# Performance work log

Hardware: AMD Instinct MI355X
Metric: run time of the kernel (lower is better)

## Reference

```python
import jax, jax.numpy as jnp
import numpy as np

B, D, LC, LQ = 64, 128, 1024, 128
NEG = -1e30


def setup_inputs() -> dict:
    key = jax.random.key(0)
    k1, k2, k3 = jax.random.split(key, 3)
    lim = float(np.sqrt(1.0 / D))
    return {
        "C": jax.random.normal(k1, (B, D, LC), dtype=jnp.float32),
        "Q": jax.random.normal(k2, (B, D, LQ), dtype=jnp.float32),
        "cmask": jnp.ones((B, LC), dtype=jnp.float32),
        "qmask": jnp.ones((B, LQ), dtype=jnp.float32),
        "w": jax.random.uniform(k3, (3 * D,), dtype=jnp.float32, minval=-lim, maxval=lim),
    }


def reference(C, Q, cmask, qmask, w):
    # C: [B, D, Lc], Q: [B, D, Lq] -> transpose to [B, L, D] as in the torch module
    Ct = jnp.swapaxes(C, 1, 2)  # [B, Lc, D]
    Qt = jnp.swapaxes(Q, 1, 2)  # [B, Lq, D]
    d = Ct.shape[-1]
    # Trilinear decomposition of the per-step concat([Qi, C, Q*C]) . w loop:
    # S[b,c,q] = Qt[b,q] . w_q + Ct[b,c] . w_c + (Ct[b,c] * w_m) . Qt[b,q]
    w_q, w_c, w_m = w[:d], w[d:2 * d], w[2 * d:]
    s_q = Qt @ w_q                                   # [B, Lq]
    s_c = Ct @ w_c                                   # [B, Lc]
    s_m = jnp.einsum("bcd,bqd->bcq", Ct * w_m, Qt)   # [B, Lc, Lq]
    S = s_m + s_c[:, :, None] + s_q[:, None, :]      # [B, Lc, Lq]

    S1 = jax.nn.softmax(S + (1.0 - qmask)[:, None, :] * NEG, axis=2)
    S2 = jax.nn.softmax(S + (1.0 - cmask)[:, :, None] * NEG, axis=1)

    A = jnp.einsum("bcq,bqd->bcd", S1, Qt)           # [B, Lc, D]
    S12 = jnp.einsum("bcq,bkq->bck", S1, S2)         # [B, Lc, Lc]
    Bt = jnp.einsum("bck,bkd->bcd", S12, Ct)         # [B, Lc, D]

    out = jnp.concatenate([Ct, A, Ct * A, Ct * Bt], axis=2)  # [B, Lc, 4D]
    # dropout is identity in eval mode
    return jnp.swapaxes(out, 1, 2)                   # [B, 4D, Lc]
```

## Files before the change

kernel.cpp:

```cpp
#include <hip/hip_runtime.h>
#include <cstdint>
#include <cstddef>

#define B_  64
#define D_  128
#define LC_ 1024
#define LQ_ 128
#define NEGV (-1e30f)
#define NINF (-3.402823466e38f)

typedef short s16x8 __attribute__((ext_vector_type(8)));
typedef float f32x4 __attribute__((ext_vector_type(4)));

__device__ __forceinline__ unsigned short f2bf(float x) {
    union { float f; unsigned u; } v; v.f = x;
    unsigned r = v.u + 0x7fffu + ((v.u >> 16) & 1u);
    return (unsigned short)(r >> 16);
}

__global__ __launch_bounds__(256) void kQ(const float* __restrict__ Q,
                                          const float* __restrict__ w,
                                          unsigned short* __restrict__ Qt,
                                          unsigned short* __restrict__ Qb,
                                          float* __restrict__ sq_g) {
    __shared__ float tile[32][33];
    __shared__ float wq_l[128];
    __shared__ float red[8][32];
    int t = threadIdx.x;
    int b = blockIdx.y, q0 = blockIdx.x * 32;
    if (t < 128) wq_l[t] = w[t];
    __syncthreads();
    float sqp = 0.f;
    int qq = t & 31, db = t >> 5;
    for (int ch = 0; ch < 4; ch++) {
#pragma unroll
        for (int i = 0; i < 4; i++) {
            int dl = db * 4 + i;
            float v = Q[((size_t)(b * D_ + ch * 32 + dl)) * LQ_ + q0 + qq];
            tile[dl][qq] = v;
            sqp += v * wq_l[ch * 32 + dl];
        }
        __syncthreads();
        {
            int q2 = t >> 3, ds = (t & 7) * 4;
            ushort4 o;
            o.x = f2bf(tile[ds + 0][q2]);
            o.y = f2bf(tile[ds + 1][q2]);
            o.z = f2bf(tile[ds + 2][q2]);
            o.w = f2bf(tile[ds + 3][q2]);
            *(ushort4*)&Qt[((size_t)(b * LQ_ + q0 + q2)) * D_ + ch * 32 + ds] = o;
        }
        {
            int d2 = t >> 3, qs = (t & 7) * 4;
            ushort4 o;
            o.x = f2bf(tile[d2][qs + 0]);
            o.y = f2bf(tile[d2][qs + 1]);
            o.z = f2bf(tile[d2][qs + 2]);
            o.w = f2bf(tile[d2][qs + 3]);
            *(ushort4*)&Qb[((size_t)(b * D_ + ch * 32 + d2)) * LQ_ + q0 + qs] = o;
        }
        __syncthreads();
    }
    red[db][qq] = sqp;
    __syncthreads();
    if (t < 32) {
        float s = 0.f;
#pragma unroll
        for (int j = 0; j < 8; j++) s += red[j][t];
        sq_g[b * LQ_ + q0 + t] = s;
    }
}

__global__ __launch_bounds__(256) void kS(const float* __restrict__ C,
                                          const unsigned short* __restrict__ Qt,
                                          const float* __restrict__ w,
                                          const float* __restrict__ sq_g,
                                          const float* __restrict__ cmask,
                                          const float* __restrict__ qmask,
                                          unsigned short* __restrict__ S1b,
                                          float* __restrict__ pmax_g,
                                          float* __restrict__ psum_g,
                                          float* __restrict__ T2p) {
    __shared__ unsigned short CW[128 * 136];
    __shared__ unsigned short Tg[128 * 136];
    __shared__ float4 red4[8][32];
    __shared__ float wc_l[128], wm_l[128], sq_l[128], cmv_l[128], qmv_l[128], sc_l[128];

    int t = threadIdx.x;
    int b = blockIdx.y, c0 = blockIdx.x * 128;

    int g = t >> 5, c4 = t & 31;
    float4 v[16];
    {
        const float4* Cb = (const float4*)(C + (size_t)b * D_ * LC_ + c0);
#pragma unroll
        for (int j = 0; j < 16; j++) {
            int d = j * 8 + g;
            v[j] = Cb[(size_t)d * (LC_ / 4) + c4];
        }
    }
    if (t < 128) {
        wc_l[t] = w[D_ + t];
        wm_l[t] = w[2 * D_ + t];
        sq_l[t] = sq_g[b * LQ_ + t];
        cmv_l[t] = (1.0f - cmask[b * LC_ + c0 + t]) * NEGV;
        qmv_l[t] = (1.0f - qmask[b * LQ_ + t]) * NEGV;
    }
    __syncthreads();

    {
        float4 scp = {0.f, 0.f, 0.f, 0.f};
#pragma unroll
        for (int j = 0; j < 16; j++) {
            int d = j * 8 + g;
            float wcv = wc_l[d], wmv = wm_l[d];
            scp.x += v[j].x * wcv;
            scp.y += v[j].y * wcv;
            scp.z += v[j].z * wcv;
            scp.w += v[j].w * wcv;
            ushort4 o;
            o.x = f2bf(v[j].x * wmv);
            o.y = f2bf(v[j].y * wmv);
            o.z = f2bf(v[j].z * wmv);
            o.w = f2bf(v[j].w * wmv);
            *(ushort4*)&CW[d * 136 + c4 * 4] = o;
        }
        red4[g][c4] = scp;
    }
    __syncthreads();
    if (t < 128) {
        float s = 0.f;
#pragma unroll
        for (int gg = 0; gg < 8; gg++) {
            const float* rp = (const float*)&red4[gg][t >> 2];
            s += rp[t & 3];
        }
        sc_l[t] = s;
    }
    __syncthreads();

    int wv = t >> 6, l = t & 63, quad = l >> 4, lp = l & 15;
    int w32 = wv * 32;
    f32x4 zero = {0.f, 0.f, 0.f, 0.f};
    f32x4 acc[2][8];
#pragma unroll
    for (int mc = 0; mc < 2; mc++)
#pragma unroll
        for (int qt = 0; qt < 8; qt++) acc[mc][qt] = zero;

#pragma unroll
    for (int ks = 0; ks < 4; ks++) {
        s16x8 a[2], bb[8];
#pragma unroll
        for (int mc = 0; mc < 2; mc++) {
            s16x8 av;
#pragma unroll
            for (int e = 0; e < 8; e++)
                av[e] = (short)CW[(ks * 32 + quad * 8 + e) * 136 + w32 + mc * 16 + lp];
            a[mc] = av;
        }
#pragma unroll
        for (int qt = 0; qt < 8; qt++)
            bb[qt] = *(const s16x8*)&Qt[((size_t)(b * LQ_ + qt * 16 + lp)) * D_ + ks * 32 + quad * 8];
#pragma unroll
        for (int mc = 0; mc < 2; mc++)
#pragma unroll
            for (int qt = 0; qt < 8; qt++)
                acc[mc][qt] = __builtin_amdgcn_mfma_f32_16x16x32_bf16(a[mc], bb[qt], acc[mc][qt], 0, 0, 0);
    }
#pragma unroll
    for (int mc = 0; mc < 2; mc++)
#pragma unroll
        for (int qt = 0; qt < 8; qt++)
#pragma unroll
            for (int i = 0; i < 4; i++)
                acc[mc][qt][i] += sc_l[w32 + mc * 16 + quad * 4 + i] + sq_l[qt * 16 + lp];

    float qmv_r[8];
#pragma unroll
    for (int qt = 0; qt < 8; qt++) qmv_r[qt] = qmv_l[qt * 16 + lp];

    float rm_r[2][4], ri_r[2][4], gs_r[2][4];
#pragma unroll
    for (int mc = 0; mc < 2; mc++)
#pragma unroll
        for (int i = 0; i < 4; i++) {
            int row = w32 + mc * 16 + quad * 4 + i;
            float m = NINF;
#pragma unroll
            for (int qt = 0; qt < 8; qt++) m = fmaxf(m, acc[mc][qt][i] + qmv_r[qt]);
#pragma unroll
            for (int off = 1; off < 16; off <<= 1) m = fmaxf(m, __shfl_xor(m, off, 64));
            float s = 0.f;
#pragma unroll
            for (int qt = 0; qt < 8; qt++) s += __expf(acc[mc][qt][i] + qmv_r[qt] - m);
#pragma unroll
            for (int off = 1; off < 16; off <<= 1) s += __shfl_xor(s, off, 64);
            rm_r[mc][i] = m;
            ri_r[mc][i] = 1.0f / s;
            gs_r[mc][i] = s * __expf(m + cmv_l[row]);
        }

    float cmv_r[2][4];
#pragma unroll
    for (int mc = 0; mc < 2; mc++)
#pragma unroll
        for (int i = 0; i < 4; i++) cmv_r[mc][i] = cmv_l[w32 + mc * 16 + quad * 4 + i];
    int chunk = blockIdx.x * 4 + wv;
#pragma unroll
    for (int qt = 0; qt < 8; qt++) {
        float cm = NINF;
#pragma unroll
        for (int mc = 0; mc < 2; mc++)
#pragma unroll
            for (int i = 0; i < 4; i++) cm = fmaxf(cm, acc[mc][qt][i] + cmv_r[mc][i]);
        cm = fmaxf(cm, __shfl_xor(cm, 16, 64));
        cm = fmaxf(cm, __shfl_xor(cm, 32, 64));
        float cs = 0.f;
#pragma unroll
        for (int mc = 0; mc < 2; mc++)
#pragma unroll
            for (int i = 0; i < 4; i++) cs += __expf(acc[mc][qt][i] + cmv_r[mc][i] - cm);
        cs += __shfl_xor(cs, 16, 64);
        cs += __shfl_xor(cs, 32, 64);
        if (l < 16) {
            pmax_g[((size_t)(b * 32 + chunk)) * LQ_ + qt * 16 + lp] = cm;
            psum_g[((size_t)(b * 32 + chunk)) * LQ_ + qt * 16 + lp] = cs;
        }
    }

    __syncthreads();
#pragma unroll
    for (int mc = 0; mc < 2; mc++)
#pragma unroll
        for (int qt = 0; qt < 8; qt++)
#pragma unroll
            for (int i = 0; i < 4; i++) {
                int row = w32 + mc * 16 + quad * 4 + i;
                int q = qt * 16 + lp;
                float s1 = __expf(acc[mc][qt][i] + qmv_r[qt] - rm_r[mc][i]) * ri_r[mc][i];
                CW[row * 136 + q] = f2bf(s1);
                Tg[q * 136 + row] = f2bf(s1 * gs_r[mc][i]);
            }
    __syncthreads();

    {
        int row = t >> 1, qh = (t & 1) * 64;
        const uint4* src = (const uint4*)&CW[row * 136 + qh];
        uint4* dst = (uint4*)&S1b[((size_t)(b * LC_ + c0 + row)) * LQ_ + qh];
#pragma unroll
        for (int j = 0; j < 8; j++) dst[j] = src[j];
    }

    f32x4 acc2[2][8];
#pragma unroll
    for (int mc = 0; mc < 2; mc++)
#pragma unroll
        for (int nt = 0; nt < 8; nt++) acc2[mc][nt] = zero;
#pragma unroll
    for (int ks = 0; ks < 4; ks++) {
        s16x8 a2[2], bb[8];
#pragma unroll
        for (int m = 0; m < 2; m++) {
            int d = w32 + m * 16 + lp;
            const float4* p = (const float4*)&C[((size_t)(b * D_ + d)) * LC_ + c0 + ks * 32 + quad * 8];
            float4 v0 = p[0], v1 = p[1];
            unsigned short* pp = (unsigned short*)&a2[m];
            pp[0] = f2bf(v0.x); pp[1] = f2bf(v0.y); pp[2] = f2bf(v0.z); pp[3] = f2bf(v0.w);
            pp[4] = f2bf(v1.x); pp[5] = f2bf(v1.y); pp[6] = f2bf(v1.z); pp[7] = f2bf(v1.w);
        }
#pragma unroll
        for (int nt = 0; nt < 8; nt++)
            bb[nt] = *(const s16x8*)&Tg[(nt * 16 + lp) * 136 + ks * 32 + quad * 8];
#pragma unroll
        for (int m = 0; m < 2; m++)
#pragma unroll
            for (int nt = 0; nt < 8; nt++)
                acc2[m][nt] = __builtin_amdgcn_mfma_f32_16x16x32_bf16(a2[m], bb[nt], acc2[m][nt], 0, 0, 0);
    }
    size_t base = ((size_t)(blockIdx.x * B_ + b)) * ((size_t)D_ * LQ_);
#pragma unroll
    for (int mc = 0; mc < 2; mc++)
#pragma unroll
        for (int i = 0; i < 4; i++) {
            int d = w32 + mc * 16 + quad * 4 + i;
#pragma unroll
            for (int nt = 0; nt < 8; nt++)
                T2p[base + (size_t)d * LQ_ + nt * 16 + lp] = acc2[mc][nt][i];
        }
}

__global__ __launch_bounds__(128) void k2b(const float* __restrict__ pmax,
                                           const float* __restrict__ psum,
                                           float* __restrict__ hq_g,
                                           float* __restrict__ ci_g) {
    int q = threadIdx.x, b = blockIdx.x;
    float m = NINF;
    for (int j = 0; j < 32; j++) m = fmaxf(m, pmax[((size_t)(b * 32 + j)) * LQ_ + q]);
    float s = 0.f;
    for (int j = 0; j < 32; j++)
        s += psum[((size_t)(b * 32 + j)) * LQ_ + q] * __expf(pmax[((size_t)(b * 32 + j)) * LQ_ + q] - m);
    hq_g[b * LQ_ + q] = __expf(-m);
    ci_g[b * LQ_ + q] = 1.0f / s;
}

__global__ __launch_bounds__(256) void k3b(const float* __restrict__ T2p,
                                           const float* __restrict__ hq_g,
                                           const float* __restrict__ ci_g,
                                           unsigned short* __restrict__ T2b) {
    int idx = blockIdx.x * 256 + threadIdx.x;
    const size_t N = (size_t)B_ * D_ * LQ_;
    int b = idx >> 14, q = idx & 127;
    float s = 0.f;
#pragma unroll
    for (int j = 0; j < 8; j++) s += T2p[(size_t)j * N + idx];
    T2b[idx] = f2bf(s * hq_g[b * LQ_ + q] * ci_g[b * LQ_ + q]);
}

__global__ __launch_bounds__(256) void kC_out(const float* __restrict__ C,
                                              const unsigned short* __restrict__ Qb,
                                              const unsigned short* __restrict__ T2b,
                                              const unsigned short* __restrict__ S1b,
                                              float* __restrict__ out) {
    int t = threadIdx.x;
    int b = blockIdx.y, c0 = blockIdx.x * 64;
    int wv = t >> 6, l = t & 63, quad = l >> 4, lp = l & 15;
    int w32 = wv * 32;
    f32x4 zero = {0.f, 0.f, 0.f, 0.f};
    f32x4 accA[2][4], accB[2][4];
#pragma unroll
    for (int mc = 0; mc < 2; mc++)
#pragma unroll
        for (int nt = 0; nt < 4; nt++) { accA[mc][nt] = zero; accB[mc][nt] = zero; }

#pragma unroll
    for (int ks = 0; ks < 4; ks++) {
        s16x8 aq[2], at[2], bb[4];
        aq[0] = *(const s16x8*)&Qb[((size_t)(b * D_ + w32 + lp)) * LQ_ + ks * 32 + quad * 8];
        aq[1] = *(const s16x8*)&Qb[((size_t)(b * D_ + w32 + 16 + lp)) * LQ_ + ks * 32 + quad * 8];
        at[0] = *(const s16x8*)&T2b[((size_t)(b * D_ + w32 + lp)) * LQ_ + ks * 32 + quad * 8];
        at[1] = *(const s16x8*)&T2b[((size_t)(b * D_ + w32 + 16 + lp)) * LQ_ + ks * 32 + quad * 8];
#pragma unroll
        for (int nt = 0; nt < 4; nt++)
            bb[nt] = *(const s16x8*)&S1b[((size_t)(b * LC_ + c0 + nt * 16 + lp)) * LQ_ + ks * 32 + quad * 8];
#pragma unroll
        for (int mc = 0; mc < 2; mc++)
#pragma unroll
            for (int nt = 0; nt < 4; nt++) {
                accA[mc][nt] = __builtin_amdgcn_mfma_f32_16x16x32_bf16(aq[mc], bb[nt], accA[mc][nt], 0, 0, 0);
                accB[mc][nt] = __builtin_amdgcn_mfma_f32_16x16x32_bf16(at[mc], bb[nt], accB[mc][nt], 0, 0, 0);
            }
    }
    const size_t DL = (size_t)D_ * LC_;
#pragma unroll
    for (int mc = 0; mc < 2; mc++)
#pragma unroll
        for (int i = 0; i < 4; i++) {
            int d = w32 + mc * 16 + quad * 4 + i;
            const float* Crow = C + ((size_t)(b * D_ + d)) * LC_ + c0;
            size_t ob = ((size_t)(b * 4 * D_ + d)) * LC_ + c0;
#pragma unroll
            for (int nt = 0; nt < 4; nt++) {
                int c = nt * 16 + lp;
                float cv = Crow[c];
                float a = accA[mc][nt][i];
                float bt = accB[mc][nt][i];
                out[ob + c] = cv;
                out[ob + DL + c] = a;
                out[ob + 2 * DL + c] = cv * a;
                out[ob + 3 * DL + c] = cv * bt;
            }
        }
}

extern "C" void kernel_launch(void* const* d_in, const int* in_sizes, int n_in,
                              void* d_out, int out_size, void* d_ws, size_t ws_size,
                              hipStream_t stream) {
    const float* C     = (const float*)d_in[0];
    const float* Q     = (const float*)d_in[1];
    const float* cmask = (const float*)d_in[2];
    const float* qmask = (const float*)d_in[3];
    const float* w     = (const float*)d_in[4];
    float* out = (float*)d_out;

    unsigned short* us = (unsigned short*)d_ws;
    unsigned short* S1b = us;
    unsigned short* Qt  = S1b + (size_t)B_ * LC_ * LQ_;
    unsigned short* Qb  = Qt  + (size_t)B_ * LQ_ * D_;
    unsigned short* T2b = Qb  + (size_t)B_ * D_ * LQ_;
    float* fp = (float*)(T2b + (size_t)B_ * D_ * LQ_);
    float* T2p    = fp;
    float* pmax_g = T2p + (size_t)8 * B_ * D_ * LQ_;
    float* psum_g = pmax_g + (size_t)B_ * 32 * LQ_;
    float* sq_g   = psum_g + (size_t)B_ * 32 * LQ_;
    float* hq_g   = sq_g + (size_t)B_ * LQ_;
    float* ci_g   = hq_g + (size_t)B_ * LQ_;

    kQ<<<dim3(LQ_ / 32, B_), 256, 0, stream>>>(Q, w, Qt, Qb, sq_g);
    kS<<<dim3(LC_ / 128, B_), 256, 0, stream>>>(C, Qt, w, sq_g, cmask, qmask,
                                                S1b, pmax_g, psum_g, T2p);
    k2b<<<dim3(B_), 128, 0, stream>>>(pmax_g, psum_g, hq_g, ci_g);
    k3b<<<dim3(B_ * D_ * LQ_ / 256), 256, 0, stream>>>(T2p, hq_g, ci_g, T2b);
    kC_out<<<dim3(LC_ / 64, B_), 256, 0, stream>>>(C, Qb, T2b, S1b, out);
}
```

Before: 241.5 us.

## Swizzle CW LDS layout, cache softmax exps, transpose output GEMM for vector stores

Applies an XOR swizzle to the CW shared-memory tile on both the write and the column-gather read, to cut LDS bank conflicts. Stores the row-softmax exponentials back into the accumulators so the exp is computed once instead of twice. Restructures kC_out so each wave owns 16 context columns across all 128 D rows, with S1 as the A operand. The MFMA output then lands as 4 consecutive c values per lane, which allows float4 loads of C and float4 stores to all four output planes. The cost is more register pressure, since each wave now holds 16 accumulators and 16 B fragments, and the wider per-lane reads of Qb and T2b.

Result: slower. 250.6 us (+3.8%).

```diff
diff --git a/kernel.cpp b/kernel.cpp
--- a/kernel.cpp
+++ b/kernel.cpp
@@ -123,7 +123,7 @@
             o.y = f2bf(v[j].y * wmv);
             o.z = f2bf(v[j].z * wmv);
             o.w = f2bf(v[j].w * wmv);
-            *(ushort4*)&CW[d * 136 + c4 * 4] = o;
+            *(ushort4*)&CW[d * 136 + ((c4 ^ (j & 7)) << 2)] = o;
         }
         red4[g][c4] = scp;
     }
@@ -151,12 +151,15 @@
 #pragma unroll
     for (int ks = 0; ks < 4; ks++) {
         s16x8 a[2], bb[8];
+        int x3 = (ks * 4 + quad) & 7;
 #pragma unroll
         for (int mc = 0; mc < 2; mc++) {
             s16x8 av;
+            int c = w32 + mc * 16 + lp;
+            int cb = ((c >> 2) ^ x3) << 2, clo = c & 3;
 #pragma unroll
             for (int e = 0; e < 8; e++)
-                av[e] = (short)CW[(ks * 32 + quad * 8 + e) * 136 + w32 + mc * 16 + lp];
+                av[e] = (short)CW[(ks * 32 + quad * 8 + e) * 136 + cb + clo];
             a[mc] = av;
         }
 #pragma unroll
@@ -179,33 +182,25 @@
     float qmv_r[8];
 #pragma unroll
     for (int qt = 0; qt < 8; qt++) qmv_r[qt] = qmv_l[qt * 16 + lp];
-
-    float rm_r[2][4], ri_r[2][4], gs_r[2][4];
+    float cmv_r[2][4];
+#pragma unroll
+    for (int mc = 0; mc < 2; mc++)
+#pragma unroll
+        for (int i = 0; i < 4; i++) cmv_r[mc][i] = cmv_l[w32 + mc * 16 + quad * 4 + i];
+
+    float rm_r[2][4];
 #pragma unroll
     for (int mc = 0; mc < 2; mc++)
 #pragma unroll
         for (int i = 0; i < 4; i++) {
-            int row = w32 + mc * 16 + quad * 4 + i;
             float m = NINF;
 #pragma unroll
             for (int qt = 0; qt < 8; qt++) m = fmaxf(m, acc[mc][qt][i] + qmv_r[qt]);
 #pragma unroll
             for (int off = 1; off < 16; off <<= 1) m = fmaxf(m, __shfl_xor(m, off, 64));
-            float s = 0.f;
-#pragma unroll
-            for (int qt = 0; qt < 8; qt++) s += __expf(acc[mc][qt][i] + qmv_r[qt] - m);
-#pragma unroll
-            for (int off = 1; off < 16; off <<= 1) s += __shfl_xor(s, off, 64);
             rm_r[mc][i] = m;
-            ri_r[mc][i] = 1.0f / s;
-            gs_r[mc][i] = s * __expf(m + cmv_l[row]);
-        }
-
-    float cmv_r[2][4];
-#pragma unroll
-    for (int mc = 0; mc < 2; mc++)
-#pragma unroll
-        for (int i = 0; i < 4; i++) cmv_r[mc][i] = cmv_l[w32 + mc * 16 + quad * 4 + i];
+        }
+
     int chunk = blockIdx.x * 4 + wv;
 #pragma unroll
     for (int qt = 0; qt < 8; qt++) {
@@ -229,6 +224,24 @@
         }
     }
 
+    float ri_r[2][4], gs_r[2][4];
+#pragma unroll
+    for (int mc = 0; mc < 2; mc++)
+#pragma unroll
+        for (int i = 0; i < 4; i++) {
+            float s = 0.f;
+#pragma unroll
+            for (int qt = 0; qt < 8; qt++) {
+                float e = __expf(acc[mc][qt][i] + qmv_r[qt] - rm_r[mc][i]);
+                acc[mc][qt][i] = e;
+                s += e;
+            }
+#pragma unroll
+            for (int off = 1; off < 16; off <<= 1) s += __shfl_xor(s, off, 64);
+            ri_r[mc][i] = 1.0f / s;
+            gs_r[mc][i] = s * __expf(rm_r[mc][i] + cmv_r[mc][i]);
+        }
+
     __syncthreads();
 #pragma unroll
     for (int mc = 0; mc < 2; mc++)
@@ -238,7 +251,7 @@
             for (int i = 0; i < 4; i++) {
                 int row = w32 + mc * 16 + quad * 4 + i;
                 int q = qt * 16 + lp;
-                float s1 = __expf(acc[mc][qt][i] + qmv_r[qt] - rm_r[mc][i]) * ri_r[mc][i];
+                float s1 = acc[mc][qt][i] * ri_r[mc][i];
                 CW[row * 136 + q] = f2bf(s1);
                 Tg[q * 136 + row] = f2bf(s1 * gs_r[mc][i]);
             }
@@ -325,52 +338,41 @@
     int t = threadIdx.x;
     int b = blockIdx.y, c0 = blockIdx.x * 64;
     int wv = t >> 6, l = t & 63, quad = l >> 4, lp = l & 15;
-    int w32 = wv * 32;
+    int cw = c0 + wv * 16;
     f32x4 zero = {0.f, 0.f, 0.f, 0.f};
-    f32x4 accA[2][4], accB[2][4];
-#pragma unroll
-    for (int mc = 0; mc < 2; mc++)
-#pragma unroll
-        for (int nt = 0; nt < 4; nt++) { accA[mc][nt] = zero; accB[mc][nt] = zero; }
+    f32x4 accA[8], accB[8];
+#pragma unroll
+    for (int nt = 0; nt < 8; nt++) { accA[nt] = zero; accB[nt] = zero; }
 
 #pragma unroll
     for (int ks = 0; ks < 4; ks++) {
-        s16x8 aq[2], at[2], bb[4];
-        aq[0] = *(const s16x8*)&Qb[((size_t)(b * D_ + w32 + lp)) * LQ_ + ks * 32 + quad * 8];
-        aq[1] = *(const s16x8*)&Qb[((size_t)(b * D_ + w32 + 16 + lp)) * LQ_ + ks * 32 + quad * 8];
-        at[0] = *(const s16x8*)&T2b[((size_t)(b * D_ + w32 + lp)) * LQ_ + ks * 32 + quad * 8];
-        at[1] = *(const s16x8*)&T2b[((size_t)(b * D_ + w32 + 16 + lp)) * LQ_ + ks * 32 + quad * 8];
-#pragma unroll
-        for (int nt = 0; nt < 4; nt++)
-            bb[nt] = *(const s16x8*)&S1b[((size_t)(b * LC_ + c0 + nt * 16 + lp)) * LQ_ + ks * 32 + quad * 8];
-#pragma unroll
-        for (int mc = 0; mc < 2; mc++)
-#pragma unroll
-            for (int nt = 0; nt < 4; nt++) {
-                accA[mc][nt] = __builtin_amdgcn_mfma_f32_16x16x32_bf16(aq[mc], bb[nt], accA[mc][nt], 0, 0, 0);
-                accB[mc][nt] = __builtin_amdgcn_mfma_f32_16x16x32_bf16(at[mc], bb[nt], accB[mc][nt], 0, 0, 0);
-            }
+        s16x8 a = *(const s16x8*)&S1b[((size_t)(b * LC_ + cw + lp)) * LQ_ + ks * 32 + quad * 8];
+        s16x8 bq[8], bt[8];
+#pragma unroll
+        for (int nt = 0; nt < 8; nt++) {
+            bq[nt] = *(const s16x8*)&Qb[((size_t)(b * D_ + nt * 16 + lp)) * LQ_ + ks * 32 + quad * 8];
+            bt[nt] = *(const s16x8*)&T2b[((size_t)(b * D_ + nt * 16 + lp)) * LQ_ + ks * 32 + quad * 8];
+        }
+#pragma unroll
+        for (int nt = 0; nt < 8; nt++) {
+            accA[nt] = __builtin_amdgcn_mfma_f32_16x16x32_bf16(a, bq[nt], accA[nt], 0, 0, 0);
+            accB[nt] = __builtin_amdgcn_mfma_f32_16x16x32_bf16(a, bt[nt], accB[nt], 0, 0, 0);
+        }
     }
     const size_t DL = (size_t)D_ * LC_;
-#pragma unroll
-    for (int mc = 0; mc < 2; mc++)
-#pragma unroll
-        for (int i = 0; i < 4; i++) {
-            int d = w32 + mc * 16 + quad * 4 + i;
-            const float* Crow = C + ((size_t)(b * D_ + d)) * LC_ + c0;
-            size_t ob = ((size_t)(b * 4 * D_ + d)) * LC_ + c0;
-#pragma unroll
-            for (int nt = 0; nt < 4; nt++) {
-                int c = nt * 16 + lp;
-                float cv = Crow[c];
-                float a = accA[mc][nt][i];
-                float bt = accB[mc][nt][i];
-                out[ob + c] = cv;
-                out[ob + DL + c] = a;
-                out[ob + 2 * DL + c] = cv * a;
-                out[ob + 3 * DL + c] = cv * bt;
-            }
-        }
+    int cc = cw + quad * 4;
+#pragma unroll
+    for (int nt = 0; nt < 8; nt++) {
+        int d = nt * 16 + lp;
+        const f32x4 cv = *(const f32x4*)&C[((size_t)(b * D_ + d)) * LC_ + cc];
+        f32x4 av = accA[nt], bv = accB[nt];
+        f32x4 ca = cv * av, cb = cv * bv;
+        size_t ob = ((size_t)(b * 4 * D_ + d)) * LC_ + cc;
+        *(f32x4*)&out[ob] = cv;
+        *(f32x4*)&out[ob + DL] = av;
+        *(f32x4*)&out[ob + 2 * DL] = ca;
+        *(f32x4*)&out[ob + 3 * DL] = cb;
+    }
 }
 
 extern "C" void kernel_launch(void* const* d_in, const int* in_sizes, int n_in,
```

## Fuse Q preprocessing into score kernel and merge reduction kernels

Applied to the files above, without the earlier changes.

The standalone Q transpose/bf16 kernel is removed: each score block now loads Q itself, transposes it through shared memory, computes s_q locally, and reuses the LDS buffers. The two small reduction kernels are merged into one that computes per-query column scales and reduces the T2 partials. The output kernel converts Q to bf16 on the fly and uses 128-column tiles. It also adds an XOR swizzle on the CW shared buffer, caches exponentials instead of recomputing them, and sets a two-blocks-per-CU launch bound. This cuts two launches and the Qt/Qb workspace traffic, at the cost of every score block redoing Q's transpose and conversion.

Measured after the change: 219.1 us. 9.3% less time.

```diff
diff --git a/kernel.cpp b/kernel.cpp
--- a/kernel.cpp
+++ b/kernel.cpp
@@ -18,78 +18,24 @@
     return (unsigned short)(r >> 16);
 }
 
-__global__ __launch_bounds__(256) void kQ(const float* __restrict__ Q,
-                                          const float* __restrict__ w,
-                                          unsigned short* __restrict__ Qt,
-                                          unsigned short* __restrict__ Qb,
-                                          float* __restrict__ sq_g) {
-    __shared__ float tile[32][33];
-    __shared__ float wq_l[128];
-    __shared__ float red[8][32];
+__global__ __launch_bounds__(256, 2) void k1(const float* __restrict__ C,
+                                             const float* __restrict__ Q,
+                                             const float* __restrict__ cmask,
+                                             const float* __restrict__ qmask,
+                                             const float* __restrict__ w,
+                                             unsigned short* __restrict__ S1b,
+                                             float* __restrict__ pmax_g,
+                                             float* __restrict__ psum_g,
+                                             float* __restrict__ T2p) {
+    __shared__ unsigned short CW[128 * 136];
+    __shared__ unsigned short QT[128 * 136];
+    __shared__ float4 red4[8][32];
+    __shared__ float wc_l[128], wm_l[128], cmv_l[128], qmv_l[128], sc_l[128], sq_l[128];
+
     int t = threadIdx.x;
-    int b = blockIdx.y, q0 = blockIdx.x * 32;
-    if (t < 128) wq_l[t] = w[t];
-    __syncthreads();
-    float sqp = 0.f;
-    int qq = t & 31, db = t >> 5;
-    for (int ch = 0; ch < 4; ch++) {
-#pragma unroll
-        for (int i = 0; i < 4; i++) {
-            int dl = db * 4 + i;
-            float v = Q[((size_t)(b * D_ + ch * 32 + dl)) * LQ_ + q0 + qq];
-            tile[dl][qq] = v;
-            sqp += v * wq_l[ch * 32 + dl];
-        }
-        __syncthreads();
-        {
-            int q2 = t >> 3, ds = (t & 7) * 4;
-            ushort4 o;
-            o.x = f2bf(tile[ds + 0][q2]);
-            o.y = f2bf(tile[ds + 1][q2]);
-            o.z = f2bf(tile[ds + 2][q2]);
-            o.w = f2bf(tile[ds + 3][q2]);
-            *(ushort4*)&Qt[((size_t)(b * LQ_ + q0 + q2)) * D_ + ch * 32 + ds] = o;
-        }
-        {
-            int d2 = t >> 3, qs = (t & 7) * 4;
-            ushort4 o;
-            o.x = f2bf(tile[d2][qs + 0]);
-            o.y = f2bf(tile[d2][qs + 1]);
-            o.z = f2bf(tile[d2][qs + 2]);
-            o.w = f2bf(tile[d2][qs + 3]);
-            *(ushort4*)&Qb[((size_t)(b * D_ + ch * 32 + d2)) * LQ_ + q0 + qs] = o;
-        }
-        __syncthreads();
-    }
-    red[db][qq] = sqp;
-    __syncthreads();
-    if (t < 32) {
-        float s = 0.f;
-#pragma unroll
-        for (int j = 0; j < 8; j++) s += red[j][t];
-        sq_g[b * LQ_ + q0 + t] = s;
-    }
-}
-
-__global__ __launch_bounds__(256) void kS(const float* __restrict__ C,
-                                          const unsigned short* __restrict__ Qt,
-                                          const float* __restrict__ w,
-                                          const float* __restrict__ sq_g,
-                                          const float* __restrict__ cmask,
-                                          const float* __restrict__ qmask,
-                                          unsigned short* __restrict__ S1b,
-                                          float* __restrict__ pmax_g,
-                                          float* __restrict__ psum_g,
-                                          float* __restrict__ T2p) {
-    __shared__ unsigned short CW[128 * 136];
-    __shared__ unsigned short Tg[128 * 136];
-    __shared__ float4 red4[8][32];
-    __shared__ float wc_l[128], wm_l[128], sq_l[128], cmv_l[128], qmv_l[128], sc_l[128];
-
-    int t = threadIdx.x;
-    int b = blockIdx.y, c0 = blockIdx.x * 128;
-
+    int b = blockIdx.y, ct = blockIdx.x, c0 = ct * 128;
     int g = t >> 5, c4 = t & 31;
+
     float4 v[16];
     {
         const float4* Cb = (const float4*)(C + (size_t)b * D_ * LC_ + c0);
@@ -99,14 +45,49 @@
             v[j] = Cb[(size_t)d * (LC_ / 4) + c4];
         }
     }
+    float* wq_l = (float*)red4;
     if (t < 128) {
+        wq_l[t] = w[t];
         wc_l[t] = w[D_ + t];
         wm_l[t] = w[2 * D_ + t];
-        sq_l[t] = sq_g[b * LQ_ + t];
         cmv_l[t] = (1.0f - cmask[b * LC_ + c0 + t]) * NEGV;
         qmv_l[t] = (1.0f - qmask[b * LQ_ + t]) * NEGV;
     }
     __syncthreads();
+
+    {
+        float* CWf = (float*)CW;
+        int qq = t >> 1, ph = t & 1;
+        float sqv = 0.f;
+#pragma unroll
+        for (int h = 0; h < 2; h++) {
+#pragma unroll
+            for (int j = 0; j < 8; j++) {
+                int idx = j * 256 + t;
+                int r = idx >> 5, cc = idx & 31;
+                float4 qv = *(const float4*)&Q[((size_t)(b * D_ + h * 64 + r)) * LQ_ + cc * 4];
+                *(float4*)&CWf[r * 132 + cc * 4] = qv;
+            }
+            __syncthreads();
+            unsigned short u[32];
+#pragma unroll
+            for (int k = 0; k < 32; k++) {
+                float val = CWf[(ph * 32 + k) * 132 + qq];
+                sqv += val * wq_l[h * 64 + ph * 32 + k];
+                u[k] = f2bf(val);
+            }
+#pragma unroll
+            for (int k4 = 0; k4 < 8; k4++) {
+                ushort4 o;
+                o.x = u[k4 * 4 + 0]; o.y = u[k4 * 4 + 1];
+                o.z = u[k4 * 4 + 2]; o.w = u[k4 * 4 + 3];
+                *(ushort4*)&QT[qq * 136 + h * 64 + ph * 32 + k4 * 4] = o;
+            }
+            __syncthreads();
+        }
+        sqv += __shfl_xor(sqv, 1, 64);
+        if (ph == 0) sq_l[qq] = sqv;
+    }
 
     {
         float4 scp = {0.f, 0.f, 0.f, 0.f};
@@ -123,7 +104,7 @@
             o.y = f2bf(v[j].y * wmv);
             o.z = f2bf(v[j].z * wmv);
             o.w = f2bf(v[j].w * wmv);
-            *(ushort4*)&CW[d * 136 + c4 * 4] = o;
+            *(ushort4*)&CW[d * 136 + ((c4 ^ (j & 7)) << 2)] = o;
         }
         red4[g][c4] = scp;
     }
@@ -151,17 +132,20 @@
 #pragma unroll
     for (int ks = 0; ks < 4; ks++) {
         s16x8 a[2], bb[8];
+        int x3 = (ks * 4 + quad) & 7;
 #pragma unroll
         for (int mc = 0; mc < 2; mc++) {
             s16x8 av;
+            int c = w32 + mc * 16 + lp;
+            int cb = ((c >> 2) ^ x3) << 2, clo = c & 3;
 #pragma unroll
             for (int e = 0; e < 8; e++)
-                av[e] = (short)CW[(ks * 32 + quad * 8 + e) * 136 + w32 + mc * 16 + lp];
+                av[e] = (short)CW[(ks * 32 + quad * 8 + e) * 136 + cb + clo];
             a[mc] = av;
         }
 #pragma unroll
         for (int qt = 0; qt < 8; qt++)
-            bb[qt] = *(const s16x8*)&Qt[((size_t)(b * LQ_ + qt * 16 + lp)) * D_ + ks * 32 + quad * 8];
+            bb[qt] = *(const s16x8*)&QT[(qt * 16 + lp) * 136 + ks * 32 + quad * 8];
 #pragma unroll
         for (int mc = 0; mc < 2; mc++)
 #pragma unroll
@@ -179,34 +163,26 @@
     float qmv_r[8];
 #pragma unroll
     for (int qt = 0; qt < 8; qt++) qmv_r[qt] = qmv_l[qt * 16 + lp];
-
-    float rm_r[2][4], ri_r[2][4], gs_r[2][4];
+    float cmv_r[2][4];
+#pragma unroll
+    for (int mc = 0; mc < 2; mc++)
+#pragma unroll
+        for (int i = 0; i < 4; i++) cmv_r[mc][i] = cmv_l[w32 + mc * 16 + quad * 4 + i];
+
+    float rm_r[2][4];
 #pragma unroll
     for (int mc = 0; mc < 2; mc++)
 #pragma unroll
         for (int i = 0; i < 4; i++) {
-            int row = w32 + mc * 16 + quad * 4 + i;
             float m = NINF;
 #pragma unroll
             for (int qt = 0; qt < 8; qt++) m = fmaxf(m, acc[mc][qt][i] + qmv_r[qt]);
 #pragma unroll
             for (int off = 1; off < 16; off <<= 1) m = fmaxf(m, __shfl_xor(m, off, 64));
-            float s = 0.f;
-#pragma unroll
-            for (int qt = 0; qt < 8; qt++) s += __expf(acc[mc][qt][i] + qmv_r[qt] - m);
-#pragma unroll
-            for (int off = 1; off < 16; off <<= 1) s += __shfl_xor(s, off, 64);
             rm_r[mc][i] = m;
-            ri_r[mc][i] = 1.0f / s;
-            gs_r[mc][i] = s * __expf(m + cmv_l[row]);
-        }
-
-    float cmv_r[2][4];
-#pragma unroll
-    for (int mc = 0; mc < 2; mc++)
-#pragma unroll
-        for (int i = 0; i < 4; i++) cmv_r[mc][i] = cmv_l[w32 + mc * 16 + quad * 4 + i];
-    int chunk = blockIdx.x * 4 + wv;
+        }
+
+    int chunk = ct * 4 + wv;
 #pragma unroll
     for (int qt = 0; qt < 8; qt++) {
         float cm = NINF;
@@ -229,6 +205,24 @@
         }
     }
 
+    float ri_r[2][4], gs_r[2][4];
+#pragma unroll
+    for (int mc = 0; mc < 2; mc++)
+#pragma unroll
+        for (int i = 0; i < 4; i++) {
+            float s = 0.f;
+#pragma unroll
+            for (int qt = 0; qt < 8; qt++) {
+                float e = __expf(acc[mc][qt][i] + qmv_r[qt] - rm_r[mc][i]);
+                acc[mc][qt][i] = e;
+                s += e;
+            }
+#pragma unroll
+            for (int off = 1; off < 16; off <<= 1) s += __shfl_xor(s, off, 64);
+            ri_r[mc][i] = 1.0f / s;
+            gs_r[mc][i] = s * __expf(rm_r[mc][i] + cmv_r[mc][i]);
+        }
+
     __syncthreads();
 #pragma unroll
     for (int mc = 0; mc < 2; mc++)
@@ -238,9 +232,9 @@
             for (int i = 0; i < 4; i++) {
                 int row = w32 + mc * 16 + quad * 4 + i;
                 int q = qt * 16 + lp;
-                float s1 = __expf(acc[mc][qt][i] + qmv_r[qt] - rm_r[mc][i]) * ri_r[mc][i];
+                float s1 = acc[mc][qt][i] * ri_r[mc][i];
                 CW[row * 136 + q] = f2bf(s1);
-                Tg[q * 136 + row] = f2bf(s1 * gs_r[mc][i]);
+                QT[q * 136 + row] = f2bf(s1 * gs_r[mc][i]);
             }
     __syncthreads();
 
@@ -271,14 +265,14 @@
         }
 #pragma unroll
         for (int nt = 0; nt < 8; nt++)
-            bb[nt] = *(const s16x8*)&Tg[(nt * 16 + lp) * 136 + ks * 32 + quad * 8];
+            bb[nt] = *(const s16x8*)&QT[(nt * 16 + lp) * 136 + ks * 32 + quad * 8];
 #pragma unroll
         for (int m = 0; m < 2; m++)
 #pragma unroll
             for (int nt = 0; nt < 8; nt++)
                 acc2[m][nt] = __builtin_amdgcn_mfma_f32_16x16x32_bf16(a2[m], bb[nt], acc2[m][nt], 0, 0, 0);
     }
-    size_t base = ((size_t)(blockIdx.x * B_ + b)) * ((size_t)D_ * LQ_);
+    size_t base = ((size_t)(ct * B_ + b)) * ((size_t)D_ * LQ_);
 #pragma unroll
     for (int mc = 0; mc < 2; mc++)
 #pragma unroll
@@ -290,63 +284,84 @@
         }
 }
 
-__global__ __launch_bounds__(128) void k2b(const float* __restrict__ pmax,
-                                           const float* __restrict__ psum,
-                                           float* __restrict__ hq_g,
-                                           float* __restrict__ ci_g) {
-    int q = threadIdx.x, b = blockIdx.x;
-    float m = NINF;
-    for (int j = 0; j < 32; j++) m = fmaxf(m, pmax[((size_t)(b * 32 + j)) * LQ_ + q]);
-    float s = 0.f;
-    for (int j = 0; j < 32; j++)
-        s += psum[((size_t)(b * 32 + j)) * LQ_ + q] * __expf(pmax[((size_t)(b * 32 + j)) * LQ_ + q] - m);
-    hq_g[b * LQ_ + q] = __expf(-m);
-    ci_g[b * LQ_ + q] = 1.0f / s;
+__global__ __launch_bounds__(256) void k2(const float* __restrict__ pmax_g,
+                                          const float* __restrict__ psum_g,
+                                          const float* __restrict__ T2p,
+                                          unsigned short* __restrict__ T2b) {
+    __shared__ float scale_l[128];
+    int t = threadIdx.x;
+    int bid = blockIdx.x;
+    int b = bid >> 3, dc = bid & 7;
+    if (t < 128) {
+        float m = NINF;
+        for (int j = 0; j < 32; j++)
+            m = fmaxf(m, pmax_g[((size_t)(b * 32 + j)) * LQ_ + t]);
+        float s = 0.f;
+        for (int j = 0; j < 32; j++)
+            s += psum_g[((size_t)(b * 32 + j)) * LQ_ + t] *
+                 __expf(pmax_g[((size_t)(b * 32 + j)) * LQ_ + t] - m);
+        scale_l[t] = __expf(-m) / s;
+    }
+    __syncthreads();
+    int d = dc * 16 + (t >> 4), q8 = (t & 15) * 8;
+    float a8[8] = {0.f, 0.f, 0.f, 0.f, 0.f, 0.f, 0.f, 0.f};
+#pragma unroll
+    for (int j = 0; j < 8; j++) {
+        const float* p = &T2p[(((size_t)j * B_ + b) * D_ + d) * LQ_ + q8];
+        float4 x0 = *(const float4*)p, x1 = *(const float4*)(p + 4);
+        a8[0] += x0.x; a8[1] += x0.y; a8[2] += x0.z; a8[3] += x0.w;
+        a8[4] += x1.x; a8[5] += x1.y; a8[6] += x1.z; a8[7] += x1.w;
+    }
+    ushort4 o0, o1;
+    o0.x = f2bf(a8[0] * scale_l[q8 + 0]);
+    o0.y = f2bf(a8[1] * scale_l[q8 + 1]);
+    o0.z = f2bf(a8[2] * scale_l[q8 + 2]);
+    o0.w = f2bf(a8[3] * scale_l[q8 + 3]);
+    o1.x = f2bf(a8[4] * scale_l[q8 + 4]);
+    o1.y = f2bf(a8[5] * scale_l[q8 + 5]);
+    o1.z = f2bf(a8[6] * scale_l[q8 + 6]);
+    o1.w = f2bf(a8[7] * scale_l[q8 + 7]);
+    size_t tb = ((size_t)(b * D_ + d)) * LQ_ + q8;
+    *(ushort4*)&T2b[tb] = o0;
+    *(ushort4*)&T2b[tb + 4] = o1;
 }
 
-__global__ __launch_bounds__(256) void k3b(const float* __restrict__ T2p,
-                                           const float* __restrict__ hq_g,
-                                           const float* __restrict__ ci_g,
-                                           unsigned short* __restrict__ T2b) {
-    int idx = blockIdx.x * 256 + threadIdx.x;
-    const size_t N = (size_t)B_ * D_ * LQ_;
-    int b = idx >> 14, q = idx & 127;
-    float s = 0.f;
-#pragma unroll
-    for (int j = 0; j < 8; j++) s += T2p[(size_t)j * N + idx];
-    T2b[idx] = f2bf(s * hq_g[b * LQ_ + q] * ci_g[b * LQ_ + q]);
-}
-
-__global__ __launch_bounds__(256) void kC_out(const float* __restrict__ C,
-                                              const unsigned short* __restrict__ Qb,
-                                              const unsigned short* __restrict__ T2b,
-                                              const unsigned short* __restrict__ S1b,
-                                              float* __restrict__ out) {
+__global__ __launch_bounds__(256) void k3(const float* __restrict__ C,
+                                          const float* __restrict__ Q,
+                                          const unsigned short* __restrict__ T2b,
+                                          const unsigned short* __restrict__ S1b,
+                                          float* __restrict__ out) {
     int t = threadIdx.x;
-    int b = blockIdx.y, c0 = blockIdx.x * 64;
+    int b = blockIdx.y, c0 = blockIdx.x * 128;
     int wv = t >> 6, l = t & 63, quad = l >> 4, lp = l & 15;
     int w32 = wv * 32;
     f32x4 zero = {0.f, 0.f, 0.f, 0.f};
-    f32x4 accA[2][4], accB[2][4];
-#pragma unroll
-    for (int mc = 0; mc < 2; mc++)
-#pragma unroll
-        for (int nt = 0; nt < 4; nt++) { accA[mc][nt] = zero; accB[mc][nt] = zero; }
+    f32x4 accA[2][8], accB[2][8];
+#pragma unroll
+    for (int mc = 0; mc < 2; mc++)
+#pragma unroll
+        for (int nt = 0; nt < 8; nt++) { accA[mc][nt] = zero; accB[mc][nt] = zero; }
 
 #pragma unroll
     for (int ks = 0; ks < 4; ks++) {
-        s16x8 aq[2], at[2], bb[4];
-        aq[0] = *(const s16x8*)&Qb[((size_t)(b * D_ + w32 + lp)) * LQ_ + ks * 32 + quad * 8];
-        aq[1] = *(const s16x8*)&Qb[((size_t)(b * D_ + w32 + 16 + lp)) * LQ_ + ks * 32 + quad * 8];
-        at[0] = *(const s16x8*)&T2b[((size_t)(b * D_ + w32 + lp)) * LQ_ + ks * 32 + quad * 8];
-        at[1] = *(const s16x8*)&T2b[((size_t)(b * D_ + w32 + 16 + lp)) * LQ_ + ks * 32 + quad * 8];
-#pragma unroll
-        for (int nt = 0; nt < 4; nt++)
+        s16x8 aq[2], at[2], bb[8];
+#pragma unroll
+        for (int mc = 0; mc < 2; mc++) {
+            int d = w32 + mc * 16 + lp;
+            const float4* p = (const float4*)&Q[((size_t)(b * D_ + d)) * LQ_ + ks * 32 + quad * 8];
+            float4 v0 = p[0], v1 = p[1];
+            unsigned short* pp = (unsigned short*)&aq[mc];
+            pp[0] = f2bf(v0.x); pp[1] = f2bf(v0.y); pp[2] = f2bf(v0.z); pp[3] = f2bf(v0.w);
+            pp[4] = f2bf(v1.x); pp[5] = f2bf(v1.y); pp[6] = f2bf(v1.z); pp[7] = f2bf(v1.w);
+            at[mc] = *(const s16x8*)&T2b[((size_t)(b * D_ + d)) * LQ_ + ks * 32 + quad * 8];
+        }
+#pragma unroll
+        for (int nt = 0; nt < 8; nt++)
             bb[nt] = *(const s16x8*)&S1b[((size_t)(b * LC_ + c0 + nt * 16 + lp)) * LQ_ + ks * 32 + quad * 8];
 #pragma unroll
         for (int mc = 0; mc < 2; mc++)
 #pragma unroll
-            for (int nt = 0; nt < 4; nt++) {
+            for (int nt = 0; nt < 8; nt++) {
                 accA[mc][nt] = __builtin_amdgcn_mfma_f32_16x16x32_bf16(aq[mc], bb[nt], accA[mc][nt], 0, 0, 0);
                 accB[mc][nt] = __builtin_amdgcn_mfma_f32_16x16x32_bf16(at[mc], bb[nt], accB[mc][nt], 0, 0, 0);
             }
@@ -360,7 +375,7 @@
             const float* Crow = C + ((size_t)(b * D_ + d)) * LC_ + c0;
             size_t ob = ((size_t)(b * 4 * D_ + d)) * LC_ + c0;
 #pragma unroll
-            for (int nt = 0; nt < 4; nt++) {
+            for (int nt = 0; nt < 8; nt++) {
                 int c = nt * 16 + lp;
                 float cv = Crow[c];
                 float a = accA[mc][nt][i];
@@ -385,21 +400,14 @@
 
     unsigned short* us = (unsigned short*)d_ws;
     unsigned short* S1b = us;
-    unsigned short* Qt  = S1b + (size_t)B_ * LC_ * LQ_;
-    unsigned short* Qb  = Qt  + (size_t)B_ * LQ_ * D_;
-    unsigned short* T2b = Qb  + (size_t)B_ * D_ * LQ_;
+    unsigned short* T2b = S1b + (size_t)B_ * LC_ * LQ_;
     float* fp = (float*)(T2b + (size_t)B_ * D_ * LQ_);
     float* T2p    = fp;
     float* pmax_g = T2p + (size_t)8 * B_ * D_ * LQ_;
     float* psum_g = pmax_g + (size_t)B_ * 32 * LQ_;
-    float* sq_g   = psum_g + (size_t)B_ * 32 * LQ_;
-    float* hq_g   = sq_g + (size_t)B_ * LQ_;
-    float* ci_g   = hq_g + (size_t)B_ * LQ_;
-
-    kQ<<<dim3(LQ_ / 32, B_), 256, 0, stream>>>(Q, w, Qt, Qb, sq_g);
-    kS<<<dim3(LC_ / 128, B_), 256, 0, stream>>>(C, Qt, w, sq_g, cmask, qmask,
+
+    k1<<<dim3(LC_ / 128, B_), 256, 0, stream>>>(C, Q, cmask, qmask, w,
                                                 S1b, pmax_g, psum_g, T2p);
-    k2b<<<dim3(B_), 128, 0, stream>>>(pmax_g, psum_g, hq_g, ci_g);
-    k3b<<<dim3(B_ * D_ * LQ_ / 256), 256, 0, stream>>>(T2p, hq_g, ci_g, T2b);
-    kC_out<<<dim3(LC_ / 64, B_), 256, 0, stream>>>(C, Qb, T2b, S1b, out);
+    k2<<<dim3(B_ * 8), 256, 0, stream>>>(pmax_g, psum_g, T2p, T2b);
+    k3<<<dim3(LC_ / 128, B_), 256, 0, stream>>>(C, Q, T2b, S1b, out);
 }
```
